# Kernel tuning notes

Measured on AMD Instinct MI355X. Metric: run time of the kernel, lower is better.

## Reference

```python
import jax, jax.numpy as jnp
import numpy as np

TOP_K = 2


def setup_inputs() -> dict:
    key = jax.random.key(0)
    k0, k1, k2, k3, k4, k5 = jax.random.split(key, 6)
    N, D_IN, D_OUT, H, G = 8192, 1024, 1024, 4096, 3
    E = 2 ** G
    x = jax.random.normal(k0, (N, D_IN), jnp.float32)
    # gate: Linear(in_dim, gate_dim, bias=False) followed by act (ReLU)
    Wg = jax.random.normal(k1, (D_IN, G), jnp.float32) * (1.0 / np.sqrt(D_IN))
    # experts: per-expert 2-layer MLP: Linear(in,hid) + ReLU + Linear(hid,out)
    W1 = jax.random.normal(k2, (E, D_IN, H), jnp.float32) * (1.0 / np.sqrt(D_IN))
    b1 = jax.random.normal(k3, (E, H), jnp.float32) * 0.01
    W2 = jax.random.normal(k4, (E, H, D_OUT), jnp.float32) * (1.0 / np.sqrt(H))
    b2 = jax.random.normal(k5, (E, D_OUT), jnp.float32) * 0.01
    return {"x": x, "Wg": Wg, "W1": W1, "b1": b1, "W2": W2, "b2": b2}


def _hypercube_mask(E, G, dtype):
    # binary(arange(2^G), G) * 2 - 1 : corners of the hypercube in {-1,+1}^G
    codes = jnp.arange(E)
    bits = (codes[:, None] >> jnp.arange(G)[None, :]) & 1  # [E, G]
    return (bits * 2 - 1).astype(dtype)


def reference(x, Wg, W1, b1, W2, b2):
    G = Wg.shape[1]
    E = W1.shape[0]
    N = x.shape[0]
    mask = _hypercube_mask(E, G, x.dtype)                 # [E, G]
    logits = jax.nn.relu(x @ Wg)                          # [N, G]
    scores = logits @ mask.T                              # [N, E] = sum_d logits*mask
    probs = jax.nn.softmax(scores, axis=1)                # softmax over experts
    topv, topi = jax.lax.top_k(probs, TOP_K)              # [N, k]
    topv = topv / topv.sum(axis=-1, keepdims=True)        # renormalize selected probs
    # dense combine weights: zero for non-selected experts (same math as gather/scatter dispatch)
    combine = jnp.zeros((N, E), x.dtype).at[jnp.arange(N)[:, None], topi].set(topv)
    out = jnp.zeros((N, W2.shape[2]), x.dtype)
    for e in range(E):  # small fixed expert count
        h = jax.nn.relu(x @ W1[e] + b1[e])                # [N, H]
        out = out + combine[:, e:e + 1] * (h @ W2[e] + b2[e])
    return out
```

## Files before the change

### kernel.cpp

```cpp
#include <hip/hip_runtime.h>

#define NTOK 8192
#define DIN  1024
#define DOUT 1024
#define HDIM 4096
#define NEXP 8
#define NPAIR (NTOK * 2)

typedef __attribute__((ext_vector_type(8))) short bf16x8;
typedef __attribute__((ext_vector_type(4))) float f32x4;

__device__ __forceinline__ unsigned short f2bf(float f) {
  union { float f; unsigned u; } v; v.f = f;
  unsigned u = v.u;
  unsigned r = (u + 0x7fffu + ((u >> 16) & 1u)) >> 16;
  return (unsigned short)r;
}

__device__ __forceinline__ void gload16(const void* g, void* l) {
  __builtin_amdgcn_global_load_lds(
      (const __attribute__((address_space(1))) unsigned int*)g,
      (__attribute__((address_space(3))) unsigned int*)l, 16, 0, 0);
}

__device__ __forceinline__ bf16x8 ds_read128(unsigned addr) {
  bf16x8 r;
  asm volatile("ds_read_b128 %0, %1" : "=&v"(r) : "v"(addr));
  return r;
}

#define LGKM4() asm volatile("s_waitcnt lgkmcnt(4)" ::: "memory")
#define LGKM0() asm volatile("s_waitcnt lgkmcnt(0)" ::: "memory")
#define VM0()   asm volatile("s_waitcnt vmcnt(0)" ::: "memory")
#define SB0()   __builtin_amdgcn_sched_barrier(0)

__global__ void gate_kernel(const float* __restrict__ x, const float* __restrict__ Wg,
                            int* __restrict__ cnt, int* __restrict__ ptok,
                            float* __restrict__ pw) {
  const int lane = threadIdx.x & 63;
  const int t = blockIdx.x * 4 + (threadIdx.x >> 6);
  const float* xr = x + (size_t)t * DIN + lane * 16;
  const float* wr = Wg + (size_t)lane * 16 * 3;
  double d0 = 0, d1 = 0, d2 = 0;
#pragma unroll
  for (int j = 0; j < 16; j++) {
    double xv = xr[j];
    d0 += xv * wr[j * 3 + 0];
    d1 += xv * wr[j * 3 + 1];
    d2 += xv * wr[j * 3 + 2];
  }
#pragma unroll
  for (int o = 32; o > 0; o >>= 1) {
    d0 += __shfl_down(d0, o);
    d1 += __shfl_down(d1, o);
    d2 += __shfl_down(d2, o);
  }
  if (lane == 0) {
    double l0 = d0 > 0 ? d0 : 0, l1 = d1 > 0 ? d1 : 0, l2 = d2 > 0 ? d2 : 0;
    double s[NEXP];
#pragma unroll
    for (int e = 0; e < NEXP; e++)
      s[e] = ((e & 1) ? l0 : -l0) + ((e & 2) ? l1 : -l1) + ((e & 4) ? l2 : -l2);
    int e0 = 0;
    for (int e = 1; e < NEXP; e++) if (s[e] > s[e0]) e0 = e;
    int e1 = -1;
    for (int e = 0; e < NEXP; e++) { if (e == e0) continue; if (e1 < 0 || s[e] > s[e1]) e1 = e; }
    double w0 = 1.0 / (1.0 + exp(s[e1] - s[e0]));
    double w1 = 1.0 - w0;
    int p0 = atomicAdd(cnt + e0, 1);
    ptok[e0 * NTOK + p0] = t; pw[e0 * NTOK + p0] = (float)w0;
    int p1 = atomicAdd(cnt + e1, 1);
    ptok[e1 * NTOK + p1] = t; pw[e1 * NTOK + p1] = (float)w1;
  }
}

__global__ void scan_kernel(const int* __restrict__ cnt, int* __restrict__ off) {
  if (threadIdx.x == 0) {
    int a = 0;
    for (int e = 0; e < NEXP; e++) { off[e] = a; a += cnt[e]; }
  }
}

__global__ void cvt_bf16_kernel(const float* __restrict__ src,
                                unsigned short* __restrict__ dst, int n) {
  int i = (blockIdx.x * 256 + threadIdx.x) * 8;
  if (i >= n) return;
  float4 a = *(const float4*)(src + i);
  float4 b = *(const float4*)(src + i + 4);
  __align__(16) unsigned short t[8] = {f2bf(a.x), f2bf(a.y), f2bf(a.z), f2bf(a.w),
                                       f2bf(b.x), f2bf(b.y), f2bf(b.z), f2bf(b.w)};
  *(uint4*)(dst + i) = *(const uint4*)t;
}

__global__ void transpose_cvt(const float* __restrict__ src,
                              unsigned short* __restrict__ dst, int K, int N) {
  __shared__ float tile[64][65];
  const size_t base = (size_t)blockIdx.z * K * N;
  const float* s = src + base;
  unsigned short* d = dst + base;
  int n0 = blockIdx.x * 64, k0 = blockIdx.y * 64;
  for (int idx = threadIdx.x; idx < 64 * 16; idx += 256) {
    int r = idx >> 4, c4 = (idx & 15) * 4;
    float4 v = *(const float4*)(s + (size_t)(k0 + r) * N + n0 + c4);
    tile[r][c4 + 0] = v.x; tile[r][c4 + 1] = v.y;
    tile[r][c4 + 2] = v.z; tile[r][c4 + 3] = v.w;
  }
  __syncthreads();
  for (int idx = threadIdx.x; idx < 64 * 8; idx += 256) {
    int nl = idx >> 3, c8 = (idx & 7) * 8;
    __align__(16) unsigned short tmp[8];
#pragma unroll
    for (int j = 0; j < 8; j++) tmp[j] = f2bf(tile[c8 + j][nl]);
    *(uint4*)(d + (size_t)(n0 + nl) * K + k0 + c8) = *(const uint4*)tmp;
  }
}


#define STG(hh, bv, kel)                                                       \
  do {                                                                         \
    unsigned db = (unsigned)(bv) * 65536u +                                    \
                  (((hh) < 2) ? (unsigned)(hh) * 16384u                        \
                              : 32768u + (unsigned)((hh) - 2) * 16384u);       \
    const unsigned short* s0 = ((hh) < 2) ? aptr[(hh) * 2] : bptr[((hh) - 2) * 2];         \
    const unsigned short* s1 = ((hh) < 2) ? aptr[(hh) * 2 + 1] : bptr[((hh) - 2) * 2 + 1]; \
    gload16(s0 + (kel), lds + db + (unsigned)tid * 16u);                       \
    gload16(s1 + (kel), lds + db + 8192u + (unsigned)tid * 16u);               \
  } while (0)

#define RD_A(qm, bb)                                                           \
  _Pragma("unroll") for (int fi = 0; fi < 4; fi++) {                           \
    areg[fi][0] = ds_read128(aoff + (bb) + (qm) * 8192u + fi * 2048u + kx0);   \
    areg[fi][1] = ds_read128(aoff + (bb) + (qm) * 8192u + fi * 2048u + kx1);   \
  }

#define RD_B(qn, breg, bb)                                                     \
  _Pragma("unroll") for (int fj = 0; fj < 2; fj++) {                           \
    breg[fj][0] = ds_read128(boff + (bb) + (qn) * 4096u + fj * 2048u + kx0);   \
    breg[fj][1] = ds_read128(boff + (bb) + (qn) * 4096u + fj * 2048u + kx1);   \
  }

#define MM(qm, qn, breg)                                                       \
  __builtin_amdgcn_s_setprio(1);                                               \
  _Pragma("unroll") for (int ks = 0; ks < 2; ks++)                             \
    _Pragma("unroll") for (int fi = 0; fi < 4; fi++)                           \
      _Pragma("unroll") for (int fj = 0; fj < 2; fj++)                         \
        acc[(qm) * 4 + fi][(qn) * 2 + fj] =                                    \
            __builtin_amdgcn_mfma_f32_16x16x32_bf16(                           \
                areg[fi][ks], breg[fj][ks], acc[(qm) * 4 + fi][(qn) * 2 + fj], \
                0, 0, 0);                                                      \
  __builtin_amdgcn_s_setprio(0);

#define KLOOP(KT)                                                              \
  STG(0, 0, 0); STG(1, 0, 0); STG(2, 0, 0); STG(3, 0, 0);                      \
  VM0();                                                                       \
  __builtin_amdgcn_s_barrier();                                                \
  for (int t = 0; t < (KT); t++) {                                             \
    const unsigned bb = (unsigned)(t & 1) * 65536u;                            \
    const int bufn = (t + 1) & 1;                                              \
    const int kel = (t + 1) * 64;                                              \
    const bool more = (t + 1 < (KT));                                          \
    RD_A(0, bb);                                                               \
    RD_B(0, b0reg, bb);                                                        \
    RD_B(1, b1reg, bb);                                                        \
    if (more) { STG(0, bufn, kel); STG(1, bufn, kel); }                        \
    LGKM4(); SB0();                                                            \
    MM(0, 0, b0reg);                                                           \
    LGKM0(); SB0();                                                            \
    MM(0, 1, b1reg);                                                           \
    RD_A(1, bb);                                                               \
    if (more) { STG(2, bufn, kel); STG(3, bufn, kel); }                        \
    LGKM0(); SB0();                                                            \
    MM(1, 1, b1reg);                                                           \
    MM(1, 0, b0reg);                                                           \
    VM0();                                                                     \
    __builtin_amdgcn_s_barrier();                                              \
  }

__global__ __launch_bounds__(512, 1) void gemm1_kernel(
    const unsigned short* __restrict__ xbf,
    const unsigned short* __restrict__ w1t,
    const float* __restrict__ b1,
    const int* __restrict__ cnt, const int* __restrict__ off,
    const int* __restrict__ ptok,
    unsigned short* __restrict__ h)
{
  extern __shared__ char lds[];
  const int bid = blockIdx.x;
  const int e = bid & 7;
  const int ce = cnt[e];
  const int idx = bid >> 3;
  const int mt = idx >> 4;
  const int nt = idx & 15;
  const int m0 = mt * 256;
  if (m0 >= ce) return;
  const int n0 = nt * 256;
  const int oe = off[e];
  const int tid = threadIdx.x;
  const int lane = tid & 63;
  const int wid = tid >> 6;
  const int wm = wid >> 2;
  const int wn = wid & 3;

  const int kofs = ((tid & 7) * 8) ^ (((tid >> 3) & 7) << 3);
  const int rth = tid >> 3;
  const unsigned short* aptr[4];
  const unsigned short* bptr[4];
  const unsigned short* wb = w1t + (size_t)e * HDIM * DIN;
#pragma unroll
  for (int i = 0; i < 4; i++) {
    int r = rth + i * 64;
    int ta = ptok[e * NTOK + min(m0 + r, ce - 1)];
    aptr[i] = xbf + (size_t)ta * DIN + kofs;
    bptr[i] = wb + (size_t)(n0 + r) * DIN + kofs;
  }

  const int fr = lane & 15;
  const int hi = lane >> 4;
  const unsigned cxor = (unsigned)((fr & 7) << 4);
  const unsigned ldsbase = (unsigned)(size_t)(void*)lds;
  const unsigned aoff = ldsbase + (unsigned)((wm * 128 + fr) * 128);
  const unsigned boff = ldsbase + 32768u + (unsigned)((wn * 64 + fr) * 128);
  const unsigned kx0 = (unsigned)((hi * 16) ^ cxor);
  const unsigned kx1 = (unsigned)((64 + hi * 16) ^ cxor);

  f32x4 acc[8][4] = {};
  bf16x8 areg[4][2], b0reg[2][2], b1reg[2][2];

  KLOOP(DIN / 64);

#pragma unroll
  for (int am = 0; am < 8; am++) {
    int rbase = wm * 128 + am * 16 + hi * 4;
#pragma unroll
    for (int r = 0; r < 4; r++) {
      int grow = m0 + rbase + r;
      if (grow >= ce) continue;
      size_t hoff = (size_t)(oe + grow) * HDIM;
#pragma unroll
      for (int an = 0; an < 4; an++) {
        int col = n0 + wn * 64 + an * 16 + fr;
        float v = acc[am][an][r] + b1[e * HDIM + col];
        h[hoff + col] = f2bf(v > 0.f ? v : 0.f);
      }
    }
  }
}

__global__ __launch_bounds__(512, 1) void gemm2_kernel(
    const unsigned short* __restrict__ h,
    const unsigned short* __restrict__ w2t,
    const float* __restrict__ b2,
    const int* __restrict__ cnt, const int* __restrict__ off,
    const int* __restrict__ ptok, const float* __restrict__ pw,
    float* __restrict__ out)
{
  extern __shared__ char lds[];
  const int bid = blockIdx.x;
  const int e = bid & 7;
  const int ce = cnt[e];
  const int idx = bid >> 3;
  const int mt = idx >> 2;
  const int nt = idx & 3;
  const int m0 = mt * 256;
  if (m0 >= ce) return;
  const int n0 = nt * 256;
  const int oe = off[e];
  const int tid = threadIdx.x;
  const int lane = tid & 63;
  const int wid = tid >> 6;
  const int wm = wid >> 2;
  const int wn = wid & 3;

  const int kofs = ((tid & 7) * 8) ^ (((tid >> 3) & 7) << 3);
  const int rth = tid >> 3;
  const unsigned short* aptr[4];
  const unsigned short* bptr[4];
  const unsigned short* wb = w2t + (size_t)e * DOUT * HDIM;
#pragma unroll
  for (int i = 0; i < 4; i++) {
    int r = rth + i * 64;
    int rc = min(m0 + r, ce - 1);
    aptr[i] = h + (size_t)(oe + rc) * HDIM + kofs;
    bptr[i] = wb + (size_t)(n0 + r) * HDIM + kofs;
  }

  const int fr = lane & 15;
  const int hi = lane >> 4;
  const unsigned cxor = (unsigned)((fr & 7) << 4);
  const unsigned ldsbase = (unsigned)(size_t)(void*)lds;
  const unsigned aoff = ldsbase + (unsigned)((wm * 128 + fr) * 128);
  const unsigned boff = ldsbase + 32768u + (unsigned)((wn * 64 + fr) * 128);
  const unsigned kx0 = (unsigned)((hi * 16) ^ cxor);
  const unsigned kx1 = (unsigned)((64 + hi * 16) ^ cxor);

  f32x4 acc[8][4] = {};
  bf16x8 areg[4][2], b0reg[2][2], b1reg[2][2];

  KLOOP(HDIM / 64);

#pragma unroll
  for (int am = 0; am < 8; am++) {
    int rbase = wm * 128 + am * 16 + hi * 4;
#pragma unroll
    for (int r = 0; r < 4; r++) {
      int grow = m0 + rbase + r;
      if (grow >= ce) continue;
      int pidx = e * NTOK + grow;
      int token = ptok[pidx];
      float w = pw[pidx];
#pragma unroll
      for (int an = 0; an < 4; an++) {
        int col = n0 + wn * 64 + an * 16 + fr;
        float v = (acc[am][an][r] + b2[e * DOUT + col]) * w;
        atomicAdd(out + (size_t)token * DOUT + col, v);
      }
    }
  }
}

extern "C" void kernel_launch(void* const* d_in, const int* in_sizes, int n_in,
                              void* d_out, int out_size, void* d_ws, size_t ws_size,
                              hipStream_t stream) {
  const float* x  = (const float*)d_in[0];
  const float* Wg = (const float*)d_in[1];
  const float* W1 = (const float*)d_in[2];
  const float* b1 = (const float*)d_in[3];
  const float* W2 = (const float*)d_in[4];
  const float* b2 = (const float*)d_in[5];
  float* out = (float*)d_out;

  char* ws = (char*)d_ws;
  size_t o = 0;
  auto nxt = [&](size_t b) { char* p = ws + o; o = (o + b + 255) & ~(size_t)255; return p; };
  int* cnt = (int*)nxt(64);
  int* off = (int*)nxt(64);
  int* ptok = (int*)nxt((size_t)NEXP * NTOK * 4);
  float* pw = (float*)nxt((size_t)NEXP * NTOK * 4);
  unsigned short* xbf = (unsigned short*)nxt((size_t)NTOK * DIN * 2);
  unsigned short* w1t = (unsigned short*)nxt((size_t)NEXP * HDIM * DIN * 2);
  unsigned short* w2t = (unsigned short*)nxt((size_t)NEXP * DOUT * HDIM * 2);
  unsigned short* hbuf = (unsigned short*)nxt((size_t)NPAIR * HDIM * 2);

  hipFuncSetAttribute((const void*)gemm1_kernel,
                      hipFuncAttributeMaxDynamicSharedMemorySize, 131072);
  hipFuncSetAttribute((const void*)gemm2_kernel,
                      hipFuncAttributeMaxDynamicSharedMemorySize, 131072);

  hipMemsetAsync(cnt, 0, 64, stream);
  hipMemsetAsync(out, 0, (size_t)NTOK * DOUT * 4, stream);

  gate_kernel<<<NTOK / 4, 256, 0, stream>>>(x, Wg, cnt, ptok, pw);
  scan_kernel<<<1, 64, 0, stream>>>(cnt, off);
  cvt_bf16_kernel<<<(NTOK * DIN / 8) / 256, 256, 0, stream>>>(x, xbf, NTOK * DIN);
  transpose_cvt<<<dim3(HDIM / 64, DIN / 64, NEXP), 256, 0, stream>>>(W1, w1t, DIN, HDIM);
  transpose_cvt<<<dim3(DOUT / 64, HDIM / 64, NEXP), 256, 0, stream>>>(W2, w2t, HDIM, DOUT);

  gemm1_kernel<<<8 * (NTOK / 256) * (HDIM / 256), 512, 131072, stream>>>(
      xbf, w1t, b1, cnt, off, ptok, hbuf);
  gemm2_kernel<<<8 * (NTOK / 256) * (DOUT / 256), 512, 131072, stream>>>(
      hbuf, w2t, b2, cnt, off, ptok, pw, out);
}
```

Measured before the change: 887.4 us.

## Pad expert groups, deepen GEMM pipeline to 4 stages, split-K gemm2

Each expert's token list is padded to a multiple of 256 rows: padded slots repeat the last token with weight zero, which removes per-row bounds checks. The GEMM main loop moves from a 2-buffer, BK=64 scheme with a full vmcnt(0) wait every step to a 4-buffer, BK=32 ring. Three tiles are loaded ahead with partial vmcnt waits, so global loads overlap compute. gemm2 is split into two K halves to double the block count, at the cost of twice as many atomicAdds into the output and some wasted compute on padded rows.

```diff
diff --git a/kernel.cpp b/kernel.cpp
--- a/kernel.cpp
+++ b/kernel.cpp
@@ -5,7 +5,8 @@
 #define DOUT 1024
 #define HDIM 4096
 #define NEXP 8
-#define NPAIR (NTOK * 2)
+#define PSTR (NTOK + 256)
+#define HROWS 18432
 
 typedef __attribute__((ext_vector_type(8))) short bf16x8;
 typedef __attribute__((ext_vector_type(4))) float f32x4;
@@ -29,9 +30,7 @@
   return r;
 }
 
-#define LGKM4() asm volatile("s_waitcnt lgkmcnt(4)" ::: "memory")
 #define LGKM0() asm volatile("s_waitcnt lgkmcnt(0)" ::: "memory")
-#define VM0()   asm volatile("s_waitcnt vmcnt(0)" ::: "memory")
 #define SB0()   __builtin_amdgcn_sched_barrier(0)
 
 __global__ void gate_kernel(const float* __restrict__ x, const float* __restrict__ Wg,
@@ -68,16 +67,32 @@
     double w0 = 1.0 / (1.0 + exp(s[e1] - s[e0]));
     double w1 = 1.0 - w0;
     int p0 = atomicAdd(cnt + e0, 1);
-    ptok[e0 * NTOK + p0] = t; pw[e0 * NTOK + p0] = (float)w0;
+    ptok[e0 * PSTR + p0] = t; pw[e0 * PSTR + p0] = (float)w0;
     int p1 = atomicAdd(cnt + e1, 1);
-    ptok[e1 * NTOK + p1] = t; pw[e1 * NTOK + p1] = (float)w1;
-  }
-}
-
-__global__ void scan_kernel(const int* __restrict__ cnt, int* __restrict__ off) {
+    ptok[e1 * PSTR + p1] = t; pw[e1 * PSTR + p1] = (float)w1;
+  }
+}
+
+__global__ void scan_kernel(const int* __restrict__ cnt, int* __restrict__ pcnt,
+                            int* __restrict__ poff) {
   if (threadIdx.x == 0) {
     int a = 0;
-    for (int e = 0; e < NEXP; e++) { off[e] = a; a += cnt[e]; }
+    for (int e = 0; e < NEXP; e++) {
+      int cp = (cnt[e] + 255) & ~255;
+      pcnt[e] = cp; poff[e] = a; a += cp;
+    }
+  }
+}
+
+__global__ void pad_kernel(const int* __restrict__ cnt, const int* __restrict__ pcnt,
+                           int* __restrict__ ptok, float* __restrict__ pw) {
+  int e = blockIdx.x;
+  int ce = cnt[e], cp = pcnt[e];
+  if (ce == 0) return;
+  int last = ptok[e * PSTR + ce - 1];
+  for (int p = ce + threadIdx.x; p < cp; p += 256) {
+    ptok[e * PSTR + p] = last;
+    pw[e * PSTR + p] = 0.f;
   }
 }
 
@@ -116,126 +131,98 @@
 }
 
 
-#define STG(hh, bv, kel)                                                       \
-  do {                                                                         \
-    unsigned db = (unsigned)(bv) * 65536u +                                    \
-                  (((hh) < 2) ? (unsigned)(hh) * 16384u                        \
-                              : 32768u + (unsigned)((hh) - 2) * 16384u);       \
-    const unsigned short* s0 = ((hh) < 2) ? aptr[(hh) * 2] : bptr[((hh) - 2) * 2];         \
-    const unsigned short* s1 = ((hh) < 2) ? aptr[(hh) * 2 + 1] : bptr[((hh) - 2) * 2 + 1]; \
-    gload16(s0 + (kel), lds + db + (unsigned)tid * 16u);                       \
-    gload16(s1 + (kel), lds + db + 8192u + (unsigned)tid * 16u);               \
+#define STAGE(tt)                                                        \
+  do {                                                                   \
+    unsigned bb2 = ((unsigned)(tt) & 3u) * 32768u;                       \
+    int kel = (tt) * 32;                                                 \
+    gload16(aptr0 + kel, dstA + bb2);                                    \
+    gload16(aptr1 + kel, dstA + bb2 + 1024u);                            \
+    gload16(bptr0 + kel, dstA + bb2 + 16384u);                           \
+    gload16(bptr1 + kel, dstA + bb2 + 16384u + 1024u);                   \
   } while (0)
 
-#define RD_A(qm, bb)                                                           \
-  _Pragma("unroll") for (int fi = 0; fi < 4; fi++) {                           \
-    areg[fi][0] = ds_read128(aoff + (bb) + (qm) * 8192u + fi * 2048u + kx0);   \
-    areg[fi][1] = ds_read128(aoff + (bb) + (qm) * 8192u + fi * 2048u + kx1);   \
-  }
-
-#define RD_B(qn, breg, bb)                                                     \
-  _Pragma("unroll") for (int fj = 0; fj < 2; fj++) {                           \
-    breg[fj][0] = ds_read128(boff + (bb) + (qn) * 4096u + fj * 2048u + kx0);   \
-    breg[fj][1] = ds_read128(boff + (bb) + (qn) * 4096u + fj * 2048u + kx1);   \
-  }
-
-#define MM(qm, qn, breg)                                                       \
-  __builtin_amdgcn_s_setprio(1);                                               \
-  _Pragma("unroll") for (int ks = 0; ks < 2; ks++)                             \
-    _Pragma("unroll") for (int fi = 0; fi < 4; fi++)                           \
-      _Pragma("unroll") for (int fj = 0; fj < 2; fj++)                         \
-        acc[(qm) * 4 + fi][(qn) * 2 + fj] =                                    \
-            __builtin_amdgcn_mfma_f32_16x16x32_bf16(                           \
-                areg[fi][ks], breg[fj][ks], acc[(qm) * 4 + fi][(qn) * 2 + fj], \
-                0, 0, 0);                                                      \
-  __builtin_amdgcn_s_setprio(0);
-
 #define KLOOP(KT)                                                              \
-  STG(0, 0, 0); STG(1, 0, 0); STG(2, 0, 0); STG(3, 0, 0);                      \
-  VM0();                                                                       \
-  __builtin_amdgcn_s_barrier();                                                \
+  STAGE(0); STAGE(1); STAGE(2);                                                \
   for (int t = 0; t < (KT); t++) {                                             \
-    const unsigned bb = (unsigned)(t & 1) * 65536u;                            \
-    const int bufn = (t + 1) & 1;                                              \
-    const int kel = (t + 1) * 64;                                              \
-    const bool more = (t + 1 < (KT));                                          \
-    RD_A(0, bb);                                                               \
-    RD_B(0, b0reg, bb);                                                        \
-    RD_B(1, b1reg, bb);                                                        \
-    if (more) { STG(0, bufn, kel); STG(1, bufn, kel); }                        \
-    LGKM4(); SB0();                                                            \
-    MM(0, 0, b0reg);                                                           \
+    if (t + 2 < (KT))      asm volatile("s_waitcnt vmcnt(8)" ::: "memory");    \
+    else if (t + 1 < (KT)) asm volatile("s_waitcnt vmcnt(4)" ::: "memory");    \
+    else                   asm volatile("s_waitcnt vmcnt(0)" ::: "memory");    \
+    __builtin_amdgcn_s_barrier();                                              \
+    if (t + 3 < (KT)) STAGE(t + 3);                                            \
+    const unsigned bb = ((unsigned)t & 3u) * 32768u;                           \
+    _Pragma("unroll") for (int am = 0; am < 8; am++)                           \
+      afr[am] = ds_read128(aoff + bb + (unsigned)am * 1024u);                  \
+    _Pragma("unroll") for (int an = 0; an < 4; an++)                           \
+      bfr[an] = ds_read128(boff + bb + (unsigned)an * 1024u);                  \
     LGKM0(); SB0();                                                            \
-    MM(0, 1, b1reg);                                                           \
-    RD_A(1, bb);                                                               \
-    if (more) { STG(2, bufn, kel); STG(3, bufn, kel); }                        \
-    LGKM0(); SB0();                                                            \
-    MM(1, 1, b1reg);                                                           \
-    MM(1, 0, b0reg);                                                           \
-    VM0();                                                                     \
-    __builtin_amdgcn_s_barrier();                                              \
-  }
+    __builtin_amdgcn_s_setprio(1);                                             \
+    _Pragma("unroll") for (int am = 0; am < 8; am++)                           \
+      _Pragma("unroll") for (int an = 0; an < 4; an++)                         \
+        acc[am][an] = __builtin_amdgcn_mfma_f32_16x16x32_bf16(                 \
+            afr[am], bfr[an], acc[am][an], 0, 0, 0);                           \
+    __builtin_amdgcn_s_setprio(0);                                             \
+    SB0();                                                                     \
+  }
+
+#define STAGE_GEOM()                                                           \
+  const int tid = threadIdx.x;                                                 \
+  const int lane = tid & 63;                                                   \
+  const int wid = tid >> 6;                                                    \
+  const int wm = wid >> 2, wn = wid & 3;                                       \
+  const int ch0 = wid * 128 + lane;       \
+  const int ch1 = ch0 + 64;                                                    \
+  const int row0 = ch0 >> 2, row1 = ch1 >> 2;                                  \
+  const int pe0 = ((ch0 & 3) ^ ((row0 >> 1) & 3)) * 8;                         \
+  const int pe1 = ((ch1 & 3) ^ ((row1 >> 1) & 3)) * 8;                         \
+  char* dstA = lds + (unsigned)(wid * 2048 + lane * 16);                       \
+  const int fr = lane & 15;                                                    \
+  const int hi = lane >> 4;                                                    \
+  const unsigned koff = (unsigned)(((hi ^ ((fr >> 1) & 3)) << 4));             \
+  const unsigned ldsbase = (unsigned)(size_t)(void*)lds;                       \
+  const unsigned aoff = ldsbase + (unsigned)((wm * 128 + fr) * 64) + koff;     \
+  const unsigned boff = ldsbase + 16384u + (unsigned)((wn * 64 + fr) * 64) + koff;
 
 __global__ __launch_bounds__(512, 1) void gemm1_kernel(
     const unsigned short* __restrict__ xbf,
     const unsigned short* __restrict__ w1t,
     const float* __restrict__ b1,
-    const int* __restrict__ cnt, const int* __restrict__ off,
+    const int* __restrict__ pcnt, const int* __restrict__ poff,
     const int* __restrict__ ptok,
     unsigned short* __restrict__ h)
 {
   extern __shared__ char lds[];
   const int bid = blockIdx.x;
   const int e = bid & 7;
-  const int ce = cnt[e];
-  const int idx = bid >> 3;
-  const int mt = idx >> 4;
-  const int nt = idx & 15;
-  const int m0 = mt * 256;
-  if (m0 >= ce) return;
-  const int n0 = nt * 256;
-  const int oe = off[e];
-  const int tid = threadIdx.x;
-  const int lane = tid & 63;
-  const int wid = tid >> 6;
-  const int wm = wid >> 2;
-  const int wn = wid & 3;
-
-  const int kofs = ((tid & 7) * 8) ^ (((tid >> 3) & 7) << 3);
-  const int rth = tid >> 3;
-  const unsigned short* aptr[4];
-  const unsigned short* bptr[4];
+  const int cp = pcnt[e];
+  const int j = bid >> 3;
+  if (j >= (cp >> 8) * 16) return;
+  const int mt = j >> 4;
+  const int nt = j & 15;
+  const int m0 = mt << 8;
+  const int n0 = nt << 8;
+  const int oe = poff[e];
+
+  STAGE_GEOM();
+
   const unsigned short* wb = w1t + (size_t)e * HDIM * DIN;
-#pragma unroll
-  for (int i = 0; i < 4; i++) {
-    int r = rth + i * 64;
-    int ta = ptok[e * NTOK + min(m0 + r, ce - 1)];
-    aptr[i] = xbf + (size_t)ta * DIN + kofs;
-    bptr[i] = wb + (size_t)(n0 + r) * DIN + kofs;
-  }
-
-  const int fr = lane & 15;
-  const int hi = lane >> 4;
-  const unsigned cxor = (unsigned)((fr & 7) << 4);
-  const unsigned ldsbase = (unsigned)(size_t)(void*)lds;
-  const unsigned aoff = ldsbase + (unsigned)((wm * 128 + fr) * 128);
-  const unsigned boff = ldsbase + 32768u + (unsigned)((wn * 64 + fr) * 128);
-  const unsigned kx0 = (unsigned)((hi * 16) ^ cxor);
-  const unsigned kx1 = (unsigned)((64 + hi * 16) ^ cxor);
+  const int ta0 = ptok[e * PSTR + m0 + row0];
+  const int ta1 = ptok[e * PSTR + m0 + row1];
+  const unsigned short* aptr0 = xbf + (size_t)ta0 * DIN + pe0;
+  const unsigned short* aptr1 = xbf + (size_t)ta1 * DIN + pe1;
+  const unsigned short* bptr0 = wb + (size_t)(n0 + row0) * DIN + pe0;
+  const unsigned short* bptr1 = wb + (size_t)(n0 + row1) * DIN + pe1;
 
   f32x4 acc[8][4] = {};
-  bf16x8 areg[4][2], b0reg[2][2], b1reg[2][2];
-
-  KLOOP(DIN / 64);
+  bf16x8 afr[8], bfr[4];
+
+  KLOOP(DIN / 32);
 
 #pragma unroll
   for (int am = 0; am < 8; am++) {
     int rbase = wm * 128 + am * 16 + hi * 4;
 #pragma unroll
     for (int r = 0; r < 4; r++) {
-      int grow = m0 + rbase + r;
-      if (grow >= ce) continue;
-      size_t hoff = (size_t)(oe + grow) * HDIM;
+      size_t hoff = (size_t)(oe + m0 + rbase + r) * HDIM;
 #pragma unroll
       for (int an = 0; an < 4; an++) {
         int col = n0 + wn * 64 + an * 16 + fr;
@@ -250,68 +237,51 @@
     const unsigned short* __restrict__ h,
     const unsigned short* __restrict__ w2t,
     const float* __restrict__ b2,
-    const int* __restrict__ cnt, const int* __restrict__ off,
+    const int* __restrict__ pcnt, const int* __restrict__ poff,
     const int* __restrict__ ptok, const float* __restrict__ pw,
     float* __restrict__ out)
 {
   extern __shared__ char lds[];
   const int bid = blockIdx.x;
   const int e = bid & 7;
-  const int ce = cnt[e];
-  const int idx = bid >> 3;
-  const int mt = idx >> 2;
-  const int nt = idx & 3;
-  const int m0 = mt * 256;
-  if (m0 >= ce) return;
-  const int n0 = nt * 256;
-  const int oe = off[e];
-  const int tid = threadIdx.x;
-  const int lane = tid & 63;
-  const int wid = tid >> 6;
-  const int wm = wid >> 2;
-  const int wn = wid & 3;
-
-  const int kofs = ((tid & 7) * 8) ^ (((tid >> 3) & 7) << 3);
-  const int rth = tid >> 3;
-  const unsigned short* aptr[4];
-  const unsigned short* bptr[4];
+  const int cp = pcnt[e];
+  const int j = bid >> 3;
+  if (j >= (cp >> 8) * 8) return;
+  const int mt = j >> 3;
+  const int r2 = j & 7;
+  const int nt = r2 >> 1;
+  const int kh = r2 & 1;
+  const int m0 = mt << 8;
+  const int n0 = nt << 8;
+  const int oe = poff[e];
+  const int kbase = kh * 2048;
+
+  STAGE_GEOM();
+
   const unsigned short* wb = w2t + (size_t)e * DOUT * HDIM;
-#pragma unroll
-  for (int i = 0; i < 4; i++) {
-    int r = rth + i * 64;
-    int rc = min(m0 + r, ce - 1);
-    aptr[i] = h + (size_t)(oe + rc) * HDIM + kofs;
-    bptr[i] = wb + (size_t)(n0 + r) * HDIM + kofs;
-  }
-
-  const int fr = lane & 15;
-  const int hi = lane >> 4;
-  const unsigned cxor = (unsigned)((fr & 7) << 4);
-  const unsigned ldsbase = (unsigned)(size_t)(void*)lds;
-  const unsigned aoff = ldsbase + (unsigned)((wm * 128 + fr) * 128);
-  const unsigned boff = ldsbase + 32768u + (unsigned)((wn * 64 + fr) * 128);
-  const unsigned kx0 = (unsigned)((hi * 16) ^ cxor);
-  const unsigned kx1 = (unsigned)((64 + hi * 16) ^ cxor);
+  const unsigned short* aptr0 = h + (size_t)(oe + m0 + row0) * HDIM + kbase + pe0;
+  const unsigned short* aptr1 = h + (size_t)(oe + m0 + row1) * HDIM + kbase + pe1;
+  const unsigned short* bptr0 = wb + (size_t)(n0 + row0) * HDIM + kbase + pe0;
+  const unsigned short* bptr1 = wb + (size_t)(n0 + row1) * HDIM + kbase + pe1;
 
   f32x4 acc[8][4] = {};
-  bf16x8 areg[4][2], b0reg[2][2], b1reg[2][2];
-
-  KLOOP(HDIM / 64);
+  bf16x8 afr[8], bfr[4];
+
+  KLOOP(2048 / 32);
 
 #pragma unroll
   for (int am = 0; am < 8; am++) {
     int rbase = wm * 128 + am * 16 + hi * 4;
 #pragma unroll
     for (int r = 0; r < 4; r++) {
-      int grow = m0 + rbase + r;
-      if (grow >= ce) continue;
-      int pidx = e * NTOK + grow;
+      int pidx = e * PSTR + m0 + rbase + r;
       int token = ptok[pidx];
       float w = pw[pidx];
+      if (w == 0.f) continue;
 #pragma unroll
       for (int an = 0; an < 4; an++) {
         int col = n0 + wn * 64 + an * 16 + fr;
-        float v = (acc[am][an][r] + b2[e * DOUT + col]) * w;
+        float v = (acc[am][an][r] + (kh == 0 ? b2[e * DOUT + col] : 0.f)) * w;
         atomicAdd(out + (size_t)token * DOUT + col, v);
       }
     }
@@ -333,13 +303,14 @@
   size_t o = 0;
   auto nxt = [&](size_t b) { char* p = ws + o; o = (o + b + 255) & ~(size_t)255; return p; };
   int* cnt = (int*)nxt(64);
-  int* off = (int*)nxt(64);
-  int* ptok = (int*)nxt((size_t)NEXP * NTOK * 4);
-  float* pw = (float*)nxt((size_t)NEXP * NTOK * 4);
+  int* pcnt = (int*)nxt(64);
+  int* poff = (int*)nxt(64);
+  int* ptok = (int*)nxt((size_t)NEXP * PSTR * 4);
+  float* pw = (float*)nxt((size_t)NEXP * PSTR * 4);
   unsigned short* xbf = (unsigned short*)nxt((size_t)NTOK * DIN * 2);
   unsigned short* w1t = (unsigned short*)nxt((size_t)NEXP * HDIM * DIN * 2);
   unsigned short* w2t = (unsigned short*)nxt((size_t)NEXP * DOUT * HDIM * 2);
-  unsigned short* hbuf = (unsigned short*)nxt((size_t)NPAIR * HDIM * 2);
+  unsigned short* hbuf = (unsigned short*)nxt((size_t)HROWS * HDIM * 2);
 
   hipFuncSetAttribute((const void*)gemm1_kernel,
                       hipFuncAttributeMaxDynamicSharedMemorySize, 131072);
@@ -350,13 +321,14 @@
   hipMemsetAsync(out, 0, (size_t)NTOK * DOUT * 4, stream);
 
   gate_kernel<<<NTOK / 4, 256, 0, stream>>>(x, Wg, cnt, ptok, pw);
-  scan_kernel<<<1, 64, 0, stream>>>(cnt, off);
+  scan_kernel<<<1, 64, 0, stream>>>(cnt, pcnt, poff);
+  pad_kernel<<<NEXP, 256, 0, stream>>>(cnt, pcnt, ptok, pw);
   cvt_bf16_kernel<<<(NTOK * DIN / 8) / 256, 256, 0, stream>>>(x, xbf, NTOK * DIN);
   transpose_cvt<<<dim3(HDIM / 64, DIN / 64, NEXP), 256, 0, stream>>>(W1, w1t, DIN, HDIM);
   transpose_cvt<<<dim3(DOUT / 64, HDIM / 64, NEXP), 256, 0, stream>>>(W2, w2t, HDIM, DOUT);
 
-  gemm1_kernel<<<8 * (NTOK / 256) * (HDIM / 256), 512, 131072, stream>>>(
-      xbf, w1t, b1, cnt, off, ptok, hbuf);
-  gemm2_kernel<<<8 * (NTOK / 256) * (DOUT / 256), 512, 131072, stream>>>(
-      hbuf, w2t, b2, cnt, off, ptok, pw, out);
-}
+  gemm1_kernel<<<8 * 33 * 16, 512, 131072, stream>>>(
+      xbf, w1t, b1, pcnt, poff, ptok, hbuf);
+  gemm2_kernel<<<8 * 33 * 8, 512, 131072, stream>>>(
+      hbuf, w2t, b2, pcnt, poff, ptok, pw, out);
+}
```

Measured after the change: 1.029 ms. 16.0% more time.
